# Kernel tuning notes

Hardware: AMD Instinct MI355X
Metric: run time of the kernel (lower is better)

Reference implementation:

```python
import jax, jax.numpy as jnp
import numpy as np

R = 4          # args.search_range
D = 2 * R + 1  # window size per axis -> D*D = 81 output channels


def setup_inputs() -> dict:
    key = jax.random.key(0)
    k1, k2 = jax.random.split(key)
    B, C, H, W = 4, 128, 64, 128
    src = jax.random.normal(k1, (B, C, H, W), dtype=jnp.float32)
    tgt = jax.random.normal(k2, (B, C, H, W), dtype=jnp.float32)
    return {"src": src, "tgt": tgt}


def reference(src, tgt):
    # Faithful to the torch code: tgt is zero-padded by R on each spatial side,
    # then for output pixel (i, j) the window indices into the PADDED tensor are
    # I in [i-R, i+R], J in [j-R, j+R]. For i < R the index is negative, which in
    # torch wraps around -> reproduce with modular indexing.
    B, C, H, W = src.shape
    tp = jnp.pad(tgt, ((0, 0), (0, 0), (R, R), (R, R)))  # [B,C,H+2R,W+2R]
    Hp, Wp = H + 2 * R, W + 2 * R
    # col_idx[dj, j] = (j - R + dj) mod Wp
    col_idx = (jnp.arange(W)[None, :] - R + jnp.arange(D)[:, None]) % Wp  # [D,W]
    outs = []
    for di in range(D):  # small fixed loop over 9 row offsets
        row_idx = (jnp.arange(H) - R + di) % Hp        # [H]
        t_rows = tp[:, :, row_idx, :]                  # [B,C,H,Wp]
        t_win = t_rows[:, :, :, col_idx]               # [B,C,H,D,W]
        # channel-dot-product per pixel and per column offset
        outs.append(jnp.einsum('bchdw,bchw->bdhw', t_win, src))
    # channel ordering k = di*D + dj matches the original double loop over (I, J)
    return jnp.concatenate(outs, axis=1)  # [B, D*D, H, W]
```

## Files before the change

### kernel.cpp

```cpp
#include <hip/hip_runtime.h>
#include <stdint.h>

#define NB 4
#define NC 128
#define NH 64
#define NW 128
#define HW (NH * NW)
#define ND 9
#define NOUT (ND * ND)
#define PLANE 16384
#define TGT_OFF ((size_t)NB * NH * PLANE)
#define TILE (ND * NW)

typedef __attribute__((ext_vector_type(8))) short short8;
typedef __attribute__((ext_vector_type(4))) float f32x4;

__device__ __forceinline__ ushort f2bf(float f) {
  uint u = __float_as_uint(f);
  u += 0x7FFFu + ((u >> 16) & 1u);
  return (ushort)(u >> 16);
}

__global__ __launch_bounds__(512, 2) void convert_kernel(const float* __restrict__ src,
                                                         const float* __restrict__ tgt,
                                                         ushort* __restrict__ ws) {
  __shared__ ushort pl[PLANE];
  const int xcd = blockIdx.x & 7;
  const int j   = blockIdx.x >> 3;
  const int b   = xcd >> 1;
  const int t   = j >> 5;
  const int row = ((xcd & 1) << 5) | (j & 31);
  const float* in = (t ? tgt : src) + (size_t)(b * NC) * HW + row * NW;
  ushort* outp = ws + (t ? TGT_OFF : 0) + (size_t)(b * NH + row) * PLANE;

#pragma unroll
  for (int i = 0; i < 8; ++i) {
    const int cell = i * 512 + threadIdx.x;
    const int c0 = (cell >> 7) << 2;
    const int w  = cell & 127;
    ushort4 e;
    e.x = f2bf(in[(size_t)(c0 + 0) * HW + w]);
    e.y = f2bf(in[(size_t)(c0 + 1) * HW + w]);
    e.z = f2bf(in[(size_t)(c0 + 2) * HW + w]);
    e.w = f2bf(in[(size_t)(c0 + 3) * HW + w]);
    *(ushort4*)&pl[(c0 >> 3) * 1024 + w * 8 + (c0 & 7)] = e;
  }
  __syncthreads();
#pragma unroll
  for (int i = 0; i < 4; ++i) {
    const int idx = i * 512 + threadIdx.x;
    *(uint4*)(outp + idx * 8) = *(const uint4*)&pl[idx * 8];
  }
}

__global__ __launch_bounds__(512, 2) void costvol_kernel(const ushort* __restrict__ ws,
                                                         float* __restrict__ out) {
  __shared__ float outlds[ND * TILE];
  const int tid  = threadIdx.x;
  const int lane = tid & 63;
  const int wave = tid >> 6;
  const int col  = lane & 15;
  const int g    = lane >> 4;

  const int xcd = blockIdx.x & 7;
  const int b   = xcd >> 1;
  const int h   = ((xcd & 1) << 5) | (blockIdx.x >> 3);

  const ushort* ap = ws + (size_t)(b * NH + h) * PLANE;
  const ushort* tb = ws + TGT_OFF + (size_t)(b * NH) * PLANE;
  const int m0 = wave << 4;

  short8 A[4];
#pragma unroll
  for (int kk = 0; kk < 4; ++kk)
    A[kk] = *(const short8*)&ap[(4 * kk + g) * 1024 + (m0 + col) * 8];

#pragma unroll
  for (int di = 0; di < ND; ++di) {
    const int y = h + di - 8;
    if (y >= 0) {
      const ushort* tp = tb + (size_t)y * PLANE;
      short8 BD[4], BS[4];
#pragma unroll
      for (int kk = 0; kk < 4; ++kk) {
        const int off = (4 * kk + g) * 1024 + (m0 + col) * 8;
        BD[kk] = *(const short8*)&tp[off];
      }
      if (wave) {
#pragma unroll
        for (int kk = 0; kk < 4; ++kk)
          BS[kk] = *(const short8*)&tp[(4 * kk + g) * 1024 + (m0 - 16 + col) * 8];
      }

      f32x4 accD = {0.f, 0.f, 0.f, 0.f};
      f32x4 accS = {0.f, 0.f, 0.f, 0.f};
#pragma unroll
      for (int kk = 0; kk < 4; ++kk)
        accD = __builtin_amdgcn_mfma_f32_16x16x32_bf16(A[kk], BD[kk], accD, 0, 0, 0);
      if (wave) {
#pragma unroll
        for (int kk = 0; kk < 4; ++kk)
          accS = __builtin_amdgcn_mfma_f32_16x16x32_bf16(A[kk], BS[kk], accS, 0, 0, 0);
      }

      float* ol = &outlds[di * TILE];
#pragma unroll
      for (int q = 0; q < 4; ++q) {
        const int row = 4 * g + q;
        const int w   = m0 + row;
        const int djd = col - row + 8;
        if (djd >= 0 && djd <= 8)
          ol[djd * NW + ((w + 4 * djd) & 127)] = accD[q];
        if (wave) {
          const int djs = col - row - 8;
          if (djs >= 0 && djs <= 8)
            ol[djs * NW + ((w + 4 * djs) & 127)] = accS[q];
        }
      }
    }
  }

  __syncthreads();

  for (int s = tid; s < ND * ND * 32; s += 512) {
    const int di = s / (ND * 32);
    const int r  = s % (ND * 32);
    const int dj = r >> 5;
    const int w  = (r & 31) << 2;
    f32x4 o = *(const f32x4*)&outlds[di * TILE + dj * NW + ((w + 4 * dj) & 127)];
    const bool vb = (h + di - 8) >= 0;
#pragma unroll
    for (int i = 0; i < 4; ++i)
      if (!vb || (w + i + dj < 8)) o[i] = 0.f;
    *(f32x4*)(out + ((size_t)((b * NOUT + di * ND + dj) * NH + h)) * NW + w) = o;
  }
}

extern "C" void kernel_launch(void* const* d_in, const int* in_sizes, int n_in,
                              void* d_out, int out_size, void* d_ws, size_t ws_size,
                              hipStream_t stream) {
  const float* src = (const float*)d_in[0];
  const float* tgt = (const float*)d_in[1];
  float* out = (float*)d_out;
  ushort* ws = (ushort*)d_ws;
  convert_kernel<<<dim3(2 * NB * NH), dim3(512), 0, stream>>>(src, tgt, ws);
  costvol_kernel<<<dim3(NB * NH), dim3(512), 0, stream>>>(ws, out);
}
```

Baseline: 91.06 us.

## Repartition cost-volume work: one wave per row offset over 4-row, 32-column tiles

Each costvol block previously handled one full output row, with 8 waves splitting the width and looping over all 9 row offsets. Now a block covers 4 rows and a 32-column quarter, with 9 waves each owning one row offset, so the shared-memory tile shrinks and is flushed once per row. The aim is to give each wave independent work and cut LDS footprint. The cost is that source rows are reloaded per wave, there are extra barriers per row, and occupancy is one block of 576 threads per CU.

```diff
diff --git a/kernel.cpp b/kernel.cpp
--- a/kernel.cpp
+++ b/kernel.cpp
@@ -8,9 +8,11 @@
 #define HW (NH * NW)
 #define ND 9
 #define NOUT (ND * ND)
+#define SH 4
+#define QW 32
 #define PLANE 16384
 #define TGT_OFF ((size_t)NB * NH * PLANE)
-#define TILE (ND * NW)
+#define OTILE (ND * 32)
 
 typedef __attribute__((ext_vector_type(8))) short short8;
 typedef __attribute__((ext_vector_type(4))) float f32x4;
@@ -53,86 +55,95 @@
   }
 }
 
-__global__ __launch_bounds__(512, 2) void costvol_kernel(const ushort* __restrict__ ws,
+__global__ __launch_bounds__(576, 1) void costvol_kernel(const ushort* __restrict__ ws,
                                                          float* __restrict__ out) {
-  __shared__ float outlds[ND * TILE];
+  __shared__ float outlds[ND * OTILE];
   const int tid  = threadIdx.x;
   const int lane = tid & 63;
   const int wave = tid >> 6;
   const int col  = lane & 15;
   const int g    = lane >> 4;
 
-  const int xcd = blockIdx.x & 7;
-  const int b   = xcd >> 1;
-  const int h   = ((xcd & 1) << 5) | (blockIdx.x >> 3);
+  const int xcd   = blockIdx.x & 7;
+  const int r     = blockIdx.x >> 3;
+  const int combo = ((r >> 4) << 3) | xcd;
+  const int b     = combo >> 2;
+  const int q     = combo & 3;
+  const int h0    = (r & 15) << 2;
+  const int w0    = q * QW;
 
-  const ushort* ap = ws + (size_t)(b * NH + h) * PLANE;
-  const ushort* tb = ws + TGT_OFF + (size_t)(b * NH) * PLANE;
-  const int m0 = wave << 4;
+  const ushort* apl = ws + (size_t)(b * NH) * PLANE;
+  const ushort* tpl = ws + TGT_OFF + (size_t)(b * NH) * PLANE;
 
-  short8 A[4];
-#pragma unroll
-  for (int kk = 0; kk < 4; ++kk)
-    A[kk] = *(const short8*)&ap[(4 * kk + g) * 1024 + (m0 + col) * 8];
+  for (int hh = 0; hh < SH; ++hh) {
+    const int h = h0 + hh;
+    const int y = h + wave - 8;
 
-#pragma unroll
-  for (int di = 0; di < ND; ++di) {
-    const int y = h + di - 8;
     if (y >= 0) {
-      const ushort* tp = tb + (size_t)y * PLANE;
-      short8 BD[4], BS[4];
+      const ushort* ap = apl + (size_t)h * PLANE;
+      const ushort* tp = tpl + (size_t)y * PLANE;
+
+      short8 A0[4], A1[4], B0[4], Bp[4], Bm[4];
 #pragma unroll
       for (int kk = 0; kk < 4; ++kk) {
-        const int off = (4 * kk + g) * 1024 + (m0 + col) * 8;
-        BD[kk] = *(const short8*)&tp[off];
+        const int ro = (4 * kk + g) * 1024;
+        A0[kk] = *(const short8*)&ap[ro + (w0 + col) * 8];
+        A1[kk] = *(const short8*)&ap[ro + (w0 + 16 + col) * 8];
+        B0[kk] = *(const short8*)&tp[ro + (w0 + col) * 8];
+        Bp[kk] = *(const short8*)&tp[ro + (w0 + 16 + col) * 8];
       }
-      if (wave) {
+      if (q) {
 #pragma unroll
         for (int kk = 0; kk < 4; ++kk)
-          BS[kk] = *(const short8*)&tp[(4 * kk + g) * 1024 + (m0 - 16 + col) * 8];
+          Bm[kk] = *(const short8*)&tp[(4 * kk + g) * 1024 + (w0 - 16 + col) * 8];
       }
 
-      f32x4 accD = {0.f, 0.f, 0.f, 0.f};
-      f32x4 accS = {0.f, 0.f, 0.f, 0.f};
+      f32x4 aD0 = {0.f,0.f,0.f,0.f}, aS0 = {0.f,0.f,0.f,0.f};
+      f32x4 aD1 = {0.f,0.f,0.f,0.f}, aS1 = {0.f,0.f,0.f,0.f};
 #pragma unroll
-      for (int kk = 0; kk < 4; ++kk)
-        accD = __builtin_amdgcn_mfma_f32_16x16x32_bf16(A[kk], BD[kk], accD, 0, 0, 0);
-      if (wave) {
+      for (int kk = 0; kk < 4; ++kk) {
+        aD0 = __builtin_amdgcn_mfma_f32_16x16x32_bf16(A0[kk], B0[kk], aD0, 0, 0, 0);
+        aS1 = __builtin_amdgcn_mfma_f32_16x16x32_bf16(A1[kk], B0[kk], aS1, 0, 0, 0);
+        aD1 = __builtin_amdgcn_mfma_f32_16x16x32_bf16(A1[kk], Bp[kk], aD1, 0, 0, 0);
+      }
+      if (q) {
 #pragma unroll
         for (int kk = 0; kk < 4; ++kk)
-          accS = __builtin_amdgcn_mfma_f32_16x16x32_bf16(A[kk], BS[kk], accS, 0, 0, 0);
+          aS0 = __builtin_amdgcn_mfma_f32_16x16x32_bf16(A0[kk], Bm[kk], aS0, 0, 0, 0);
       }
 
-      float* ol = &outlds[di * TILE];
+      float* ol = &outlds[wave * OTILE];
 #pragma unroll
-      for (int q = 0; q < 4; ++q) {
-        const int row = 4 * g + q;
-        const int w   = m0 + row;
+      for (int qr = 0; qr < 4; ++qr) {
+        const int row = 4 * g + qr;
         const int djd = col - row + 8;
-        if (djd >= 0 && djd <= 8)
-          ol[djd * NW + ((w + 4 * djd) & 127)] = accD[q];
-        if (wave) {
-          const int djs = col - row - 8;
-          if (djs >= 0 && djs <= 8)
-            ol[djs * NW + ((w + 4 * djs) & 127)] = accS[q];
+        const int djs = col - row - 8;
+        if (djd >= 0 && djd <= 8) {
+          ol[djd * 32 + ((row + 4 * djd) & 31)]      = aD0[qr];
+          ol[djd * 32 + ((16 + row + 4 * djd) & 31)] = aD1[qr];
+        }
+        if (djs >= 0 && djs <= 8) {
+          ol[djs * 32 + ((row + 4 * djs) & 31)]      = aS0[qr];
+          ol[djs * 32 + ((16 + row + 4 * djs) & 31)] = aS1[qr];
         }
       }
     }
-  }
+    __syncthreads();
 
-  __syncthreads();
-
-  for (int s = tid; s < ND * ND * 32; s += 512) {
-    const int di = s / (ND * 32);
-    const int r  = s % (ND * 32);
-    const int dj = r >> 5;
-    const int w  = (r & 31) << 2;
-    f32x4 o = *(const f32x4*)&outlds[di * TILE + dj * NW + ((w + 4 * dj) & 127)];
-    const bool vb = (h + di - 8) >= 0;
+    for (int s = tid; s < ND * ND * 8; s += 576) {
+      const int di = s / 72;
+      const int rr = s % 72;
+      const int dj = rr >> 3;
+      const int w4 = (rr & 7) << 2;
+      f32x4 o = *(const f32x4*)&outlds[di * OTILE + dj * 32 + ((w4 + 4 * dj) & 31)];
+      const bool vb = (h + di - 8) >= 0;
+      const int wg = w0 + w4;
 #pragma unroll
-    for (int i = 0; i < 4; ++i)
-      if (!vb || (w + i + dj < 8)) o[i] = 0.f;
-    *(f32x4*)(out + ((size_t)((b * NOUT + di * ND + dj) * NH + h)) * NW + w) = o;
+      for (int i = 0; i < 4; ++i)
+        if (!vb || (wg + i + dj < 8)) o[i] = 0.f;
+      *(f32x4*)(out + ((size_t)((b * NOUT + di * ND + dj) * NH + h)) * NW + wg) = o;
+    }
+    __syncthreads();
   }
 }
 
@@ -144,5 +155,5 @@
   float* out = (float*)d_out;
   ushort* ws = (ushort*)d_ws;
   convert_kernel<<<dim3(2 * NB * NH), dim3(512), 0, stream>>>(src, tgt, ws);
-  costvol_kernel<<<dim3(NB * NH), dim3(512), 0, stream>>>(ws, out);
+  costvol_kernel<<<dim3(NB * NH), dim3(576), 0, stream>>>(ws, out);
 }
```

New measurement: 89.96 us. No clear change (-1.2%).
